# Performance work log

Hardware: AMD Instinct MI355X
Metric: run time of the kernel (lower is better)

Reference implementation:

```python
import jax, jax.numpy as jnp
import numpy as np

NN, D, H = 100000, 300, 1024   # nodes, embedding dim, hidden dim
NG, NS = 50000, 25000          # global vocab, sense vocab
B, T = 8, 128                  # batch, sequence length (state carried across all B*T steps)


def setup_inputs() -> dict:
    key = jax.random.key(0)
    ks = jax.random.split(key, 24)
    s = lambda i, shape: (jax.random.normal(ks[i], shape, jnp.float32) * 0.02)
    return {
        "x_idx": jax.random.randint(ks[0], (B, T), 0, NN),
        "X": jax.random.normal(ks[1], (NN, D), jnp.float32) * 0.1,
        "W_z_1": s(2, (D, H)), "U_z_1": s(3, (H, H)),
        "W_r_1": s(4, (D, H)), "U_r_1": s(5, (H, H)),
        "W_1": s(6, (D, H)), "b_W_1": jnp.zeros((H,), jnp.float32),
        "U_1": s(7, (H, H)), "b_U_1": jnp.zeros((H,), jnp.float32),
        "W_z_2": s(8, (H, H)), "U_z_2": s(9, (H, H)),
        "W_r_2": s(10, (H, H)), "U_r_2": s(11, (H, H)),
        "W_2": s(12, (H, H)), "b_W_2": jnp.zeros((H,), jnp.float32),
        "U_2": s(13, (H, H)), "b_U_2": jnp.zeros((H,), jnp.float32),
        "W_g": s(14, (H, NG)), "b_g": jnp.zeros((NG,), jnp.float32),
        "W_s": s(15, (H, NS)), "b_s": jnp.zeros((NS,), jnp.float32),
    }


def reference(x_idx, X, W_z_1, U_z_1, W_r_1, U_r_1, W_1, b_W_1, U_1, b_U_1,
              W_z_2, U_z_2, W_r_2, U_r_2, W_2, b_W_2, U_2, b_U_2,
              W_g, b_g, W_s, b_s):
    # The original loops over every sample of every sequence, carrying memory_h1/h2
    # across the whole batch; only X[x_indices[0]] feeds the GRU (the GAT-projected
    # neighbours are computed but never used). Dropout in eval mode = identity.
    idx = x_idx.reshape(-1)          # [S] flattened step order (seq-major per sample)
    emb = X[idx]                     # [S, D] currentword embeddings

    def step(carry, e):
        h1, h2 = carry
        z1 = jax.nn.sigmoid(e @ W_z_1 + h1 @ U_z_1)
        r1 = jax.nn.sigmoid(e @ W_r_1 + h1 @ U_r_1)
        ht1 = jnp.tanh((e @ W_1 + b_W_1) + ((r1 * h1) @ U_1 + b_U_1))
        h1n = z1 * ht1 + (1.0 - z1) * h1
        z2 = jax.nn.sigmoid(h1n @ W_z_2 + h2 @ U_z_2)
        r2 = jax.nn.sigmoid(h1n @ W_r_2 + h2 @ U_r_2)
        ht2 = jnp.tanh((h1n @ W_2 + b_W_2) + ((r2 * h2) @ U_2 + b_U_2))
        h2n = z2 * ht2 + (1.0 - z2) * h2
        return (h1n, h2n), h2n

    h0 = jnp.zeros((H,), emb.dtype)
    _, hs = jax.lax.scan(step, (h0, h0), emb)        # hs: [S, H]
    logp_g = jax.nn.log_softmax(hs @ W_g + b_g, axis=-1)   # [S, NG]
    logp_s = jax.nn.log_softmax(hs @ W_s + b_s, axis=-1)   # [S, NS]
    return logp_g, logp_s
```

## Files before the change

### kernel.cpp

```cpp
#include <hip/hip_runtime.h>

typedef __attribute__((ext_vector_type(4))) float f32x4;
typedef __attribute__((ext_vector_type(8))) __bf16 bf16x8;
typedef __attribute__((ext_vector_type(4))) unsigned short u16x4;

#define GPAD 40
#define KEEPF(x) asm volatile("" : "+v"(x))
#define PHYS(i) ((i) + (((i) >> 6) << 2))

__device__ unsigned long long g_h1s[1025 * 1024];
__device__ unsigned long long g_rh1[1024];
__device__ unsigned long long g_h2cur[1024];
__device__ unsigned long long g_rh2[1024];
__device__ float g_ExW[1024 * 3072];
__device__ float g_hs2[1024 * 1024];

__device__ __forceinline__ unsigned short f2bf(float x) {
  unsigned u = __builtin_bit_cast(unsigned, x);
  u += 0x7FFFu + ((u >> 16) & 1u);
  return (unsigned short)(u >> 16);
}
__device__ __forceinline__ unsigned long long packtv(unsigned tag, float v) {
  return ((unsigned long long)tag << 32) | (unsigned long long)__builtin_bit_cast(unsigned, v);
}
__device__ __forceinline__ unsigned long long aload(const unsigned long long* p) {
  return __hip_atomic_load(p, __ATOMIC_RELAXED, __HIP_MEMORY_SCOPE_AGENT);
}
__device__ __forceinline__ void astore(unsigned long long* p, unsigned long long v) {
  __hip_atomic_store(p, v, __ATOMIC_RELAXED, __HIP_MEMORY_SCOPE_AGENT);
}
__device__ __forceinline__ float lo32(unsigned long long v) {
  return __builtin_bit_cast(float, (unsigned)v);
}

__global__ void init_kernel() {
  int t = threadIdx.x;
  astore(&g_rh1[t], 0ull);
  astore(&g_h2cur[t], 0ull);
  astore(&g_rh2[t], 0ull);
}

__global__ __launch_bounds__(256, 1) void fused_scan(
    const float* __restrict__ ExW,
    const float* __restrict__ Uz1, const float* __restrict__ Ur1,
    const float* __restrict__ Uw1, const float* __restrict__ bU1,
    const float* __restrict__ Wz2, const float* __restrict__ Wr2,
    const float* __restrict__ Ww2,
    const float* __restrict__ Uz2, const float* __restrict__ Ur2,
    const float* __restrict__ Uw2,
    const float* __restrict__ bW2, const float* __restrict__ bU2,
    float* __restrict__ hs2)
{
  const int tid = threadIdx.x;
  const int wv = tid >> 6, inw = tid & 63;
  __shared__ __align__(16) float h_s[1088];
  __shared__ __align__(16) float rh_s[1088];
  __shared__ __align__(16) float x_s[1088];

  if (blockIdx.x < 64) {
    const int g = blockIdx.x;
    const int c2 = inw >> 4, q = inw & 15;
    const int j = g * 16 + wv * 4 + c2;
    float uz[64], ur[64], uw[64];
#pragma unroll
    for (int i = 0; i < 64; ++i) uz[i] = Uz1[(size_t)(q * 64 + i) * 1024 + j];
#pragma unroll
    for (int i = 0; i < 64; ++i) ur[i] = Ur1[(size_t)(q * 64 + i) * 1024 + j];
#pragma unroll
    for (int i = 0; i < 64; ++i) uw[i] = Uw1[(size_t)(q * 64 + i) * 1024 + j];
#pragma unroll
    for (int i = 0; i < 64; ++i) { KEEPF(uz[i]); KEEPF(ur[i]); KEEPF(uw[i]); }
    const float bu = bU1[j];

    float xz = 0.f, xr = 0.f, xw = 0.f;
    if (q == 0) { xz = ExW[j]; xr = ExW[1024 + j]; xw = ExW[2048 + j]; }

    float zreg = 0.f, hold = 0.f;
    for (int s = 0; s < 1024; ++s) {
      {
        const unsigned long long* sl = g_h1s + (size_t)s * 1024 + tid * 4;
        unsigned long long a0, a1, a2, a3;
        for (;;) {
          a0 = aload(sl); a1 = aload(sl + 1); a2 = aload(sl + 2); a3 = aload(sl + 3);
          unsigned bad = ((unsigned)(a0 >> 32) ^ (unsigned)s) | ((unsigned)(a1 >> 32) ^ (unsigned)s) |
                         ((unsigned)(a2 >> 32) ^ (unsigned)s) | ((unsigned)(a3 >> 32) ^ (unsigned)s);
          if (bad == 0u) break;
          __builtin_amdgcn_s_sleep(1);
        }
        f32x4 v; v.x = lo32(a0); v.y = lo32(a1); v.z = lo32(a2); v.w = lo32(a3);
        *(f32x4*)&h_s[PHYS(tid * 4)] = v;
      }
      __syncthreads();
      if (q == 0) hold = h_s[PHYS(j)];
      float ar_ = 0.f;
      {
        const float* hp = h_s + q * 68;
#pragma unroll
        for (int i2 = 0; i2 < 16; ++i2) {
          f32x4 hv = *(const f32x4*)(hp + i2 * 4);
          ar_ = fmaf(ur[i2 * 4 + 0], hv.x, ar_); ar_ = fmaf(ur[i2 * 4 + 1], hv.y, ar_);
          ar_ = fmaf(ur[i2 * 4 + 2], hv.z, ar_); ar_ = fmaf(ur[i2 * 4 + 3], hv.w, ar_);
        }
      }
      ar_ += __shfl_xor(ar_, 1, 64); ar_ += __shfl_xor(ar_, 2, 64);
      ar_ += __shfl_xor(ar_, 4, 64); ar_ += __shfl_xor(ar_, 8, 64);
      if (q == 0) {
        float r = 1.f / (1.f + __expf(-(ar_ + xr)));
        astore(&g_rh1[j], packtv((unsigned)(s + 1), r * hold));
      }
      float az_ = 0.f;
      {
        const float* hp = h_s + q * 68;
#pragma unroll
        for (int i2 = 0; i2 < 16; ++i2) {
          f32x4 hv = *(const f32x4*)(hp + i2 * 4);
          az_ = fmaf(uz[i2 * 4 + 0], hv.x, az_); az_ = fmaf(uz[i2 * 4 + 1], hv.y, az_);
          az_ = fmaf(uz[i2 * 4 + 2], hv.z, az_); az_ = fmaf(uz[i2 * 4 + 3], hv.w, az_);
        }
      }
      az_ += __shfl_xor(az_, 1, 64); az_ += __shfl_xor(az_, 2, 64);
      az_ += __shfl_xor(az_, 4, 64); az_ += __shfl_xor(az_, 8, 64);
      if (q == 0) zreg = 1.f / (1.f + __expf(-(az_ + xz)));
      float nxz = 0.f, nxr = 0.f, nxw = 0.f;
      if (q == 0 && s < 1023) {
        nxz = ExW[(s + 1) * 3072 + j];
        nxr = ExW[(s + 1) * 3072 + 1024 + j];
        nxw = ExW[(s + 1) * 3072 + 2048 + j];
      }
      {
        const unsigned long long* sl = g_rh1 + tid * 4;
        unsigned long long a0, a1, a2, a3;
        const unsigned tg = (unsigned)(s + 1);
        for (;;) {
          a0 = aload(sl); a1 = aload(sl + 1); a2 = aload(sl + 2); a3 = aload(sl + 3);
          unsigned bad = ((unsigned)(a0 >> 32) ^ tg) | ((unsigned)(a1 >> 32) ^ tg) |
                         ((unsigned)(a2 >> 32) ^ tg) | ((unsigned)(a3 >> 32) ^ tg);
          if (bad == 0u) break;
          __builtin_amdgcn_s_sleep(1);
        }
        f32x4 v; v.x = lo32(a0); v.y = lo32(a1); v.z = lo32(a2); v.w = lo32(a3);
        *(f32x4*)&rh_s[PHYS(tid * 4)] = v;
      }
      __syncthreads();
      float aw_ = 0.f;
      {
        const float* rp = rh_s + q * 68;
#pragma unroll
        for (int i2 = 0; i2 < 16; ++i2) {
          f32x4 rv = *(const f32x4*)(rp + i2 * 4);
          aw_ = fmaf(uw[i2 * 4 + 0], rv.x, aw_); aw_ = fmaf(uw[i2 * 4 + 1], rv.y, aw_);
          aw_ = fmaf(uw[i2 * 4 + 2], rv.z, aw_); aw_ = fmaf(uw[i2 * 4 + 3], rv.w, aw_);
        }
      }
      aw_ += __shfl_xor(aw_, 1, 64); aw_ += __shfl_xor(aw_, 2, 64);
      aw_ += __shfl_xor(aw_, 4, 64); aw_ += __shfl_xor(aw_, 8, 64);
      if (q == 0) {
        float ht = tanhf(aw_ + xw + bu);
        float hn = zreg * ht + (1.f - zreg) * hold;
        astore(&g_h1s[(size_t)(s + 1) * 1024 + j], packtv((unsigned)(s + 1), hn));
      }
      xz = nxz; xr = nxr; xw = nxw;
    }
  } else {
    const int g = blockIdx.x - 64;
    const int c2 = inw >> 5, q = inw & 31;
    const int j = g * 8 + wv * 2 + c2;
    const int sb = q * 32 + ((q >> 1) << 2);
    float uz[32], ur[32], uw[32], wz[32], wr[32], ww[32];
#pragma unroll
    for (int i = 0; i < 32; ++i) uz[i] = Uz2[(size_t)(q * 32 + i) * 1024 + j];
#pragma unroll
    for (int i = 0; i < 32; ++i) ur[i] = Ur2[(size_t)(q * 32 + i) * 1024 + j];
#pragma unroll
    for (int i = 0; i < 32; ++i) uw[i] = Uw2[(size_t)(q * 32 + i) * 1024 + j];
#pragma unroll
    for (int i = 0; i < 32; ++i) wz[i] = Wz2[(size_t)(q * 32 + i) * 1024 + j];
#pragma unroll
    for (int i = 0; i < 32; ++i) wr[i] = Wr2[(size_t)(q * 32 + i) * 1024 + j];
#pragma unroll
    for (int i = 0; i < 32; ++i) ww[i] = Ww2[(size_t)(q * 32 + i) * 1024 + j];
#pragma unroll
    for (int i = 0; i < 32; ++i) {
      KEEPF(uz[i]); KEEPF(ur[i]); KEEPF(uw[i]);
      KEEPF(wz[i]); KEEPF(wr[i]); KEEPF(ww[i]);
    }
    const float bu = bW2[j] + bU2[j];

    float zreg = 0.f, hold = 0.f;
    for (int s = 0; s < 1024; ++s) {
      {
        const unsigned long long* sh = g_h2cur + tid * 4;
        const unsigned long long* sx = g_h1s + (size_t)(s + 1) * 1024 + tid * 4;
        unsigned long long a0, a1, a2, a3, b0, b1, b2, b3;
        const unsigned tg = (unsigned)(s + 1);
        for (;;) {
          a0 = aload(sh); a1 = aload(sh + 1); a2 = aload(sh + 2); a3 = aload(sh + 3);
          b0 = aload(sx); b1 = aload(sx + 1); b2 = aload(sx + 2); b3 = aload(sx + 3);
          unsigned bad = ((unsigned)(a0 >> 32) ^ (unsigned)s) | ((unsigned)(a1 >> 32) ^ (unsigned)s) |
                         ((unsigned)(a2 >> 32) ^ (unsigned)s) | ((unsigned)(a3 >> 32) ^ (unsigned)s) |
                         ((unsigned)(b0 >> 32) ^ tg) | ((unsigned)(b1 >> 32) ^ tg) |
                         ((unsigned)(b2 >> 32) ^ tg) | ((unsigned)(b3 >> 32) ^ tg);
          if (bad == 0u) break;
          __builtin_amdgcn_s_sleep(1);
        }
        f32x4 v; v.x = lo32(a0); v.y = lo32(a1); v.z = lo32(a2); v.w = lo32(a3);
        *(f32x4*)&h_s[PHYS(tid * 4)] = v;
        f32x4 u4; u4.x = lo32(b0); u4.y = lo32(b1); u4.z = lo32(b2); u4.w = lo32(b3);
        *(f32x4*)&x_s[PHYS(tid * 4)] = u4;
      }
      __syncthreads();
      if (q == 0) hold = h_s[PHYS(j)];
      float ar_ = 0.f;
      {
        const float* hp = h_s + sb;
        const float* xp = x_s + sb;
#pragma unroll
        for (int i2 = 0; i2 < 8; ++i2) {
          f32x4 hv = *(const f32x4*)(hp + i2 * 4);
          f32x4 xv = *(const f32x4*)(xp + i2 * 4);
          ar_ = fmaf(ur[i2 * 4 + 0], hv.x, ar_); ar_ = fmaf(ur[i2 * 4 + 1], hv.y, ar_);
          ar_ = fmaf(ur[i2 * 4 + 2], hv.z, ar_); ar_ = fmaf(ur[i2 * 4 + 3], hv.w, ar_);
          ar_ = fmaf(wr[i2 * 4 + 0], xv.x, ar_); ar_ = fmaf(wr[i2 * 4 + 1], xv.y, ar_);
          ar_ = fmaf(wr[i2 * 4 + 2], xv.z, ar_); ar_ = fmaf(wr[i2 * 4 + 3], xv.w, ar_);
        }
      }
      ar_ += __shfl_xor(ar_, 1, 64); ar_ += __shfl_xor(ar_, 2, 64);
      ar_ += __shfl_xor(ar_, 4, 64); ar_ += __shfl_xor(ar_, 8, 64);
      ar_ += __shfl_xor(ar_, 16, 64);
      if (q == 0) {
        float r = 1.f / (1.f + __expf(-ar_));
        astore(&g_rh2[j], packtv((unsigned)(s + 1), r * hold));
      }
      float az_ = 0.f;
      {
        const float* hp = h_s + sb;
        const float* xp = x_s + sb;
#pragma unroll
        for (int i2 = 0; i2 < 8; ++i2) {
          f32x4 hv = *(const f32x4*)(hp + i2 * 4);
          f32x4 xv = *(const f32x4*)(xp + i2 * 4);
          az_ = fmaf(uz[i2 * 4 + 0], hv.x, az_); az_ = fmaf(uz[i2 * 4 + 1], hv.y, az_);
          az_ = fmaf(uz[i2 * 4 + 2], hv.z, az_); az_ = fmaf(uz[i2 * 4 + 3], hv.w, az_);
          az_ = fmaf(wz[i2 * 4 + 0], xv.x, az_); az_ = fmaf(wz[i2 * 4 + 1], xv.y, az_);
          az_ = fmaf(wz[i2 * 4 + 2], xv.z, az_); az_ = fmaf(wz[i2 * 4 + 3], xv.w, az_);
        }
      }
      az_ += __shfl_xor(az_, 1, 64); az_ += __shfl_xor(az_, 2, 64);
      az_ += __shfl_xor(az_, 4, 64); az_ += __shfl_xor(az_, 8, 64);
      az_ += __shfl_xor(az_, 16, 64);
      if (q == 0) zreg = 1.f / (1.f + __expf(-az_));
      {
        const unsigned long long* sl = g_rh2 + tid * 4;
        unsigned long long a0, a1, a2, a3;
        const unsigned tg = (unsigned)(s + 1);
        for (;;) {
          a0 = aload(sl); a1 = aload(sl + 1); a2 = aload(sl + 2); a3 = aload(sl + 3);
          unsigned bad = ((unsigned)(a0 >> 32) ^ tg) | ((unsigned)(a1 >> 32) ^ tg) |
                         ((unsigned)(a2 >> 32) ^ tg) | ((unsigned)(a3 >> 32) ^ tg);
          if (bad == 0u) break;
          __builtin_amdgcn_s_sleep(1);
        }
        f32x4 v; v.x = lo32(a0); v.y = lo32(a1); v.z = lo32(a2); v.w = lo32(a3);
        *(f32x4*)&rh_s[PHYS(tid * 4)] = v;
      }
      __syncthreads();
      float aw_ = 0.f;
      {
        const float* rp = rh_s + sb;
        const float* xp = x_s + sb;
#pragma unroll
        for (int i2 = 0; i2 < 8; ++i2) {
          f32x4 rv = *(const f32x4*)(rp + i2 * 4);
          f32x4 xv = *(const f32x4*)(xp + i2 * 4);
          aw_ = fmaf(uw[i2 * 4 + 0], rv.x, aw_); aw_ = fmaf(uw[i2 * 4 + 1], rv.y, aw_);
          aw_ = fmaf(uw[i2 * 4 + 2], rv.z, aw_); aw_ = fmaf(uw[i2 * 4 + 3], rv.w, aw_);
          aw_ = fmaf(ww[i2 * 4 + 0], xv.x, aw_); aw_ = fmaf(ww[i2 * 4 + 1], xv.y, aw_);
          aw_ = fmaf(ww[i2 * 4 + 2], xv.z, aw_); aw_ = fmaf(ww[i2 * 4 + 3], xv.w, aw_);
        }
      }
      aw_ += __shfl_xor(aw_, 1, 64); aw_ += __shfl_xor(aw_, 2, 64);
      aw_ += __shfl_xor(aw_, 4, 64); aw_ += __shfl_xor(aw_, 8, 64);
      aw_ += __shfl_xor(aw_, 16, 64);
      if (q == 0) {
        float ht = tanhf(aw_ + bu);
        float hn = zreg * ht + (1.f - zreg) * hold;
        astore(&g_h2cur[j], packtv((unsigned)(s + 1), hn));
        hs2[(size_t)s * 1024 + j] = hn;
      }
    }
  }
}

__global__ __launch_bounds__(256, 1) void gemm_mfma(
    const float* __restrict__ A, const int* __restrict__ gidx, int lda,
    const float* __restrict__ B, int ldb,
    const float* __restrict__ bias,
    float* __restrict__ C, int ldc, int N, int K)
{
  __shared__ unsigned short As[128 * GPAD];
  __shared__ unsigned short Bs[128 * GPAD];
  const int tid = threadIdx.x;
  const int lane = tid & 63;
  const int wv = tid >> 6;
  const int wm = wv >> 1, wn = wv & 1;
  const int mbase = blockIdx.y * 128, nbase = blockIdx.x * 128;

  f32x4 acc[4][4];
#pragma unroll
  for (int i = 0; i < 4; ++i)
#pragma unroll
    for (int qq = 0; qq < 4; ++qq) acc[i][qq] = (f32x4){0.f, 0.f, 0.f, 0.f};

  const int ar = tid >> 1, ak = (tid & 1) * 16;
  const float* Arow;
  {
    int m = mbase + ar;
    long long gr = gidx ? (long long)gidx[m] : (long long)m;
    Arow = A + (size_t)gr * (size_t)lda;
  }
  const int bn = (tid >> 3) * 4;
  const int bk = (tid & 7) * 4;
  const bool nedge = (nbase + 128 > N);

  const int ksteps = (K + 31) >> 5;
  for (int ks = 0; ks < ksteps; ++ks) {
    const int k0 = ks << 5;
    __syncthreads();
    {
      float v[16];
      const int kg = k0 + ak;
      if (kg + 16 <= K) {
#pragma unroll
        for (int qq = 0; qq < 4; ++qq) {
          f32x4 t = *(const f32x4*)(Arow + kg + qq * 4);
          v[qq * 4 + 0] = t.x; v[qq * 4 + 1] = t.y; v[qq * 4 + 2] = t.z; v[qq * 4 + 3] = t.w;
        }
      } else {
#pragma unroll
        for (int i = 0; i < 16; ++i) v[i] = (kg + i < K) ? Arow[kg + i] : 0.f;
      }
#pragma unroll
      for (int qq = 0; qq < 4; ++qq) {
        u16x4 wq;
        wq.x = f2bf(v[qq * 4 + 0]); wq.y = f2bf(v[qq * 4 + 1]);
        wq.z = f2bf(v[qq * 4 + 2]); wq.w = f2bf(v[qq * 4 + 3]);
        *(u16x4*)&As[ar * GPAD + ak + qq * 4] = wq;
      }
    }
    {
      float bv[4][4];
#pragma unroll
      for (int kk = 0; kk < 4; ++kk) {
        int kglob = k0 + bk + kk;
        if (kglob < K) {
          if (!nedge) {
            f32x4 t = *(const f32x4*)(B + (size_t)kglob * (size_t)ldb + nbase + bn);
            bv[kk][0] = t.x; bv[kk][1] = t.y; bv[kk][2] = t.z; bv[kk][3] = t.w;
          } else {
#pragma unroll
            for (int nn = 0; nn < 4; ++nn) {
              int n = nbase + bn + nn;
              bv[kk][nn] = (n < N) ? B[(size_t)kglob * (size_t)ldb + n] : 0.f;
            }
          }
        } else {
          bv[kk][0] = bv[kk][1] = bv[kk][2] = bv[kk][3] = 0.f;
        }
      }
#pragma unroll
      for (int nn = 0; nn < 4; ++nn) {
        u16x4 wq;
        wq.x = f2bf(bv[0][nn]); wq.y = f2bf(bv[1][nn]);
        wq.z = f2bf(bv[2][nn]); wq.w = f2bf(bv[3][nn]);
        *(u16x4*)&Bs[(bn + nn) * GPAD + bk] = wq;
      }
    }
    __syncthreads();
    bf16x8 af[4], bfr[4];
    const int fr = lane & 15, fk = (lane >> 4) * 8;
#pragma unroll
    for (int mf = 0; mf < 4; ++mf)
      af[mf] = *(const bf16x8*)&As[(wm * 64 + mf * 16 + fr) * GPAD + fk];
#pragma unroll
    for (int nf = 0; nf < 4; ++nf)
      bfr[nf] = *(const bf16x8*)&Bs[(wn * 64 + nf * 16 + fr) * GPAD + fk];
#pragma unroll
    for (int mf = 0; mf < 4; ++mf)
#pragma unroll
      for (int nf = 0; nf < 4; ++nf)
        acc[mf][nf] = __builtin_amdgcn_mfma_f32_16x16x32_bf16(af[mf], bfr[nf], acc[mf][nf], 0, 0, 0);
  }
  const int fr = lane & 15, fq = lane >> 4;
#pragma unroll
  for (int nf = 0; nf < 4; ++nf) {
    int col = nbase + wn * 64 + nf * 16 + fr;
    if (col < N) {
      float bb = bias ? bias[col] : 0.f;
#pragma unroll
      for (int mf = 0; mf < 4; ++mf) {
        int row0 = mbase + wm * 64 + mf * 16 + fq * 4;
#pragma unroll
        for (int r = 0; r < 4; ++r)
          C[(size_t)(row0 + r) * (size_t)ldc + col] = acc[mf][nf][r] + bb;
      }
    }
  }
}

__global__ __launch_bounds__(256, 1) void logsoftmax_kernel(float* __restrict__ out) {
  const int row = blockIdx.x;
  float* p; int len;
  if (row < 1024) { p = out + (size_t)row * 50000u; len = 50000; }
  else            { p = out + 51200000ull + (size_t)(row - 1024) * 25000u; len = 25000; }
  const int tid = threadIdx.x;
  __shared__ float mred[4], sred[4];

  float m = -3.4e38f;
  for (int i = tid * 4; i < len; i += 1024) {
    f32x4 v = *(const f32x4*)(p + i);
    m = fmaxf(m, fmaxf(fmaxf(v.x, v.y), fmaxf(v.z, v.w)));
  }
#pragma unroll
  for (int off = 32; off >= 1; off >>= 1) m = fmaxf(m, __shfl_xor(m, off, 64));
  if ((tid & 63) == 0) mred[tid >> 6] = m;
  __syncthreads();
  m = fmaxf(fmaxf(mred[0], mred[1]), fmaxf(mred[2], mred[3]));

  float ssum = 0.f;
  for (int i = tid * 4; i < len; i += 1024) {
    f32x4 v = *(const f32x4*)(p + i);
    ssum += __expf(v.x - m) + __expf(v.y - m) + __expf(v.z - m) + __expf(v.w - m);
  }
#pragma unroll
  for (int off = 32; off >= 1; off >>= 1) ssum += __shfl_xor(ssum, off, 64);
  if ((tid & 63) == 0) sred[tid >> 6] = ssum;
  __syncthreads();
  const float lse = m + logf(sred[0] + sred[1] + sred[2] + sred[3]);

  for (int i = tid * 4; i < len; i += 1024) {
    f32x4 v = *(const f32x4*)(p + i);
    v.x -= lse; v.y -= lse; v.z -= lse; v.w -= lse;
    *(f32x4*)(p + i) = v;
  }
}

extern "C" void kernel_launch(void* const* d_in, const int* in_sizes, int n_in,
                              void* d_out, int out_size, void* d_ws, size_t ws_size,
                              hipStream_t stream) {
  (void)in_sizes; (void)n_in; (void)out_size; (void)d_ws; (void)ws_size;
  const int*   x_idx = (const int*)  d_in[0];
  const float* X     = (const float*)d_in[1];
  const float* W_z_1 = (const float*)d_in[2];
  const float* U_z_1 = (const float*)d_in[3];
  const float* W_r_1 = (const float*)d_in[4];
  const float* U_r_1 = (const float*)d_in[5];
  const float* W_1   = (const float*)d_in[6];
  const float* b_W_1 = (const float*)d_in[7];
  const float* U_1   = (const float*)d_in[8];
  const float* b_U_1 = (const float*)d_in[9];
  const float* W_z_2 = (const float*)d_in[10];
  const float* U_z_2 = (const float*)d_in[11];
  const float* W_r_2 = (const float*)d_in[12];
  const float* U_r_2 = (const float*)d_in[13];
  const float* W_2   = (const float*)d_in[14];
  const float* b_W_2 = (const float*)d_in[15];
  const float* U_2   = (const float*)d_in[16];
  const float* b_U_2 = (const float*)d_in[17];
  const float* W_g   = (const float*)d_in[18];
  const float* b_g   = (const float*)d_in[19];
  const float* W_s   = (const float*)d_in[20];
  const float* b_s   = (const float*)d_in[21];
  float* out = (float*)d_out;

  float *ExW, *hs2;
  unsigned long long* h1s;
  hipGetSymbolAddress((void**)&ExW, HIP_SYMBOL(g_ExW));
  hipGetSymbolAddress((void**)&hs2, HIP_SYMBOL(g_hs2));
  hipGetSymbolAddress((void**)&h1s, HIP_SYMBOL(g_h1s));

  const dim3 blk(256);

  init_kernel<<<dim3(1), dim3(1024), 0, stream>>>();
  hipMemsetAsync(h1s, 0, 1025ull * 1024 * sizeof(unsigned long long), stream);

  gemm_mfma<<<dim3(8, 8), blk, 0, stream>>>(X, x_idx, 300, W_z_1, 1024, nullptr, ExW + 0,    3072, 1024, 300);
  gemm_mfma<<<dim3(8, 8), blk, 0, stream>>>(X, x_idx, 300, W_r_1, 1024, nullptr, ExW + 1024, 3072, 1024, 300);
  gemm_mfma<<<dim3(8, 8), blk, 0, stream>>>(X, x_idx, 300, W_1,   1024, b_W_1,   ExW + 2048, 3072, 1024, 300);

  fused_scan<<<dim3(192), blk, 0, stream>>>(
      ExW, U_z_1, U_r_1, U_1, b_U_1,
      W_z_2, W_r_2, W_2, U_z_2, U_r_2, U_2, b_W_2, b_U_2, hs2);

  gemm_mfma<<<dim3(391, 8), blk, 0, stream>>>(hs2, nullptr, 1024, W_g, 50000, b_g, out,              50000, 50000, 1024);
  gemm_mfma<<<dim3(196, 8), blk, 0, stream>>>(hs2, nullptr, 1024, W_s, 25000, b_s, out + 51200000ll, 25000, 25000, 1024);
  logsoftmax_kernel<<<dim3(2048), blk, 0, stream>>>(out);
}
```

Measured before the change: 6.803 ms.

## Gate scan phases on sharded per-wave completion counters instead of tag polling

Adds sharded global counters per phase that each wave increments after publishing its outputs. Consumers spin on a single counter per lane with __all before reading the tagged data, rather than polling the tagged arrays directly. Because the counters gate access, the large memset of the h1 history buffer is dropped and only row 0 is zeroed in init. The next-step ExW prefetch is moved after publishing h1. This is meant to cut polling traffic on the critical path and remove the memset, at the cost of extra atomics and waitcnt stalls per step.

```diff
diff --git a/kernel.cpp b/kernel.cpp
--- a/kernel.cpp
+++ b/kernel.cpp
@@ -7,11 +7,17 @@
 #define GPAD 40
 #define KEEPF(x) asm volatile("" : "+v"(x))
 #define PHYS(i) ((i) + (((i) >> 6) << 2))
+
+#define PH_H1  0
+#define PH_RH1 1
+#define PH_H2  2
+#define PH_RH2 3
 
 __device__ unsigned long long g_h1s[1025 * 1024];
 __device__ unsigned long long g_rh1[1024];
 __device__ unsigned long long g_h2cur[1024];
 __device__ unsigned long long g_rh2[1024];
+__device__ unsigned g_cnt[4 * 32 * 16];
 __device__ float g_ExW[1024 * 3072];
 __device__ float g_hs2[1024 * 1024];
 
@@ -29,8 +35,35 @@
 __device__ __forceinline__ void astore(unsigned long long* p, unsigned long long v) {
   __hip_atomic_store(p, v, __ATOMIC_RELAXED, __HIP_MEMORY_SCOPE_AGENT);
 }
+__device__ __forceinline__ unsigned cload(const unsigned* p) {
+  return __hip_atomic_load(p, __ATOMIC_RELAXED, __HIP_MEMORY_SCOPE_AGENT);
+}
 __device__ __forceinline__ float lo32(unsigned long long v) {
   return __builtin_bit_cast(float, (unsigned)v);
+}
+
+__device__ __forceinline__ void gate(int ph, unsigned thr, int inw) {
+  const unsigned* cp = &g_cnt[(ph * 32 + (inw & 31)) * 16];
+  for (;;) {
+    unsigned v = cload(cp);
+    if (__all((int)(v >= thr))) break;
+    __builtin_amdgcn_s_sleep(1);
+  }
+}
+__device__ __forceinline__ void gate2(int phA, unsigned thrA, int phB, unsigned thrB, int inw) {
+  const unsigned* ca = &g_cnt[(phA * 32 + (inw & 31)) * 16];
+  const unsigned* cb = &g_cnt[(phB * 32 + (inw & 31)) * 16];
+  for (;;) {
+    unsigned va = cload(ca), vb = cload(cb);
+    if (__all((int)((va >= thrA) && (vb >= thrB)))) break;
+    __builtin_amdgcn_s_sleep(1);
+  }
+}
+__device__ __forceinline__ void publish_done(int ph, int wid) {
+  asm volatile("s_waitcnt vmcnt(0)" ::: "memory");
+  if ((threadIdx.x & 63) == 0)
+    (void)__hip_atomic_fetch_add(&g_cnt[(ph * 32 + (wid & 31)) * 16], 1u,
+                                 __ATOMIC_RELAXED, __HIP_MEMORY_SCOPE_AGENT);
 }
 
 __global__ void init_kernel() {
@@ -38,6 +71,9 @@
   astore(&g_rh1[t], 0ull);
   astore(&g_h2cur[t], 0ull);
   astore(&g_rh2[t], 0ull);
+  astore(&g_h1s[t], 0ull);
+  __hip_atomic_store(&g_cnt[2 * t], 0u, __ATOMIC_RELAXED, __HIP_MEMORY_SCOPE_AGENT);
+  __hip_atomic_store(&g_cnt[2 * t + 1], 0u, __ATOMIC_RELAXED, __HIP_MEMORY_SCOPE_AGENT);
 }
 
 __global__ __launch_bounds__(256, 1) void fused_scan(
@@ -59,6 +95,7 @@
 
   if (blockIdx.x < 64) {
     const int g = blockIdx.x;
+    const int wid = g * 4 + wv;
     const int c2 = inw >> 4, q = inw & 15;
     const int j = g * 16 + wv * 4 + c2;
     float uz[64], ur[64], uw[64];
@@ -77,6 +114,7 @@
 
     float zreg = 0.f, hold = 0.f;
     for (int s = 0; s < 1024; ++s) {
+      gate(PH_H1, (unsigned)s << 3, inw);
       {
         const unsigned long long* sl = g_h1s + (size_t)s * 1024 + tid * 4;
         unsigned long long a0, a1, a2, a3;
@@ -108,6 +146,7 @@
         float r = 1.f / (1.f + __expf(-(ar_ + xr)));
         astore(&g_rh1[j], packtv((unsigned)(s + 1), r * hold));
       }
+      publish_done(PH_RH1, wid);
       float az_ = 0.f;
       {
         const float* hp = h_s + q * 68;
@@ -121,12 +160,7 @@
       az_ += __shfl_xor(az_, 1, 64); az_ += __shfl_xor(az_, 2, 64);
       az_ += __shfl_xor(az_, 4, 64); az_ += __shfl_xor(az_, 8, 64);
       if (q == 0) zreg = 1.f / (1.f + __expf(-(az_ + xz)));
-      float nxz = 0.f, nxr = 0.f, nxw = 0.f;
-      if (q == 0 && s < 1023) {
-        nxz = ExW[(s + 1) * 3072 + j];
-        nxr = ExW[(s + 1) * 3072 + 1024 + j];
-        nxw = ExW[(s + 1) * 3072 + 2048 + j];
-      }
+      gate(PH_RH1, (unsigned)(s + 1) << 3, inw);
       {
         const unsigned long long* sl = g_rh1 + tid * 4;
         unsigned long long a0, a1, a2, a3;
@@ -159,10 +193,18 @@
         float hn = zreg * ht + (1.f - zreg) * hold;
         astore(&g_h1s[(size_t)(s + 1) * 1024 + j], packtv((unsigned)(s + 1), hn));
       }
+      publish_done(PH_H1, wid);
+      float nxz = 0.f, nxr = 0.f, nxw = 0.f;
+      if (q == 0 && s < 1023) {
+        nxz = ExW[(s + 1) * 3072 + j];
+        nxr = ExW[(s + 1) * 3072 + 1024 + j];
+        nxw = ExW[(s + 1) * 3072 + 2048 + j];
+      }
       xz = nxz; xr = nxr; xw = nxw;
     }
   } else {
     const int g = blockIdx.x - 64;
+    const int wid = g * 4 + wv;
     const int c2 = inw >> 5, q = inw & 31;
     const int j = g * 8 + wv * 2 + c2;
     const int sb = q * 32 + ((q >> 1) << 2);
@@ -188,6 +230,7 @@
 
     float zreg = 0.f, hold = 0.f;
     for (int s = 0; s < 1024; ++s) {
+      gate2(PH_H2, (unsigned)s << 4, PH_H1, (unsigned)(s + 1) << 3, inw);
       {
         const unsigned long long* sh = g_h2cur + tid * 4;
         const unsigned long long* sx = g_h1s + (size_t)(s + 1) * 1024 + tid * 4;
@@ -231,6 +274,7 @@
         float r = 1.f / (1.f + __expf(-ar_));
         astore(&g_rh2[j], packtv((unsigned)(s + 1), r * hold));
       }
+      publish_done(PH_RH2, wid);
       float az_ = 0.f;
       {
         const float* hp = h_s + sb;
@@ -249,6 +293,7 @@
       az_ += __shfl_xor(az_, 4, 64); az_ += __shfl_xor(az_, 8, 64);
       az_ += __shfl_xor(az_, 16, 64);
       if (q == 0) zreg = 1.f / (1.f + __expf(-az_));
+      gate(PH_RH2, (unsigned)(s + 1) << 4, inw);
       {
         const unsigned long long* sl = g_rh2 + tid * 4;
         unsigned long long a0, a1, a2, a3;
@@ -287,6 +332,7 @@
         astore(&g_h2cur[j], packtv((unsigned)(s + 1), hn));
         hs2[(size_t)s * 1024 + j] = hn;
       }
+      publish_done(PH_H2, wid);
     }
   }
 }
@@ -473,15 +519,12 @@
   float* out = (float*)d_out;
 
   float *ExW, *hs2;
-  unsigned long long* h1s;
   hipGetSymbolAddress((void**)&ExW, HIP_SYMBOL(g_ExW));
   hipGetSymbolAddress((void**)&hs2, HIP_SYMBOL(g_hs2));
-  hipGetSymbolAddress((void**)&h1s, HIP_SYMBOL(g_h1s));
 
   const dim3 blk(256);
 
   init_kernel<<<dim3(1), dim3(1024), 0, stream>>>();
-  hipMemsetAsync(h1s, 0, 1025ull * 1024 * sizeof(unsigned long long), stream);
 
   gemm_mfma<<<dim3(8, 8), blk, 0, stream>>>(X, x_idx, 300, W_z_1, 1024, nullptr, ExW + 0,    3072, 1024, 300);
   gemm_mfma<<<dim3(8, 8), blk, 0, stream>>>(X, x_idx, 300, W_r_1, 1024, nullptr, ExW + 1024, 3072, 1024, 300);
```

After: 12.82 ms. 88.5% more time.

## Replicate recurrent state into per-block mailboxes to localize spin-wait polling

Applied to the files above, without the earlier changes.

Each producer now writes its hidden-state and reset-gated values into a separate mailbox copy for every consumer block. Consumers therefore poll a private contiguous slot instead of all blocks hammering one shared array. The aim is to cut cache-line contention and coherence traffic in the cross-block handshake that runs on every recurrent step. The cost is 64–128x more atomic stores per step, a larger zero-init memset, and the next-step ExW prefetch moving to after the publish; layer-2 sleep duration is also raised.

```diff
diff --git a/kernel.cpp b/kernel.cpp
--- a/kernel.cpp
+++ b/kernel.cpp
@@ -8,12 +8,15 @@
 #define KEEPF(x) asm volatile("" : "+v"(x))
 #define PHYS(i) ((i) + (((i) >> 6) << 2))
 
+__device__ unsigned long long g_mb[384 * 1024];
 __device__ unsigned long long g_h1s[1025 * 1024];
-__device__ unsigned long long g_rh1[1024];
-__device__ unsigned long long g_h2cur[1024];
-__device__ unsigned long long g_rh2[1024];
 __device__ float g_ExW[1024 * 3072];
 __device__ float g_hs2[1024 * 1024];
+
+#define MB_H1  0
+#define MB_RH1 (64 * 1024)
+#define MB_H2  (128 * 1024)
+#define MB_RH2 (256 * 1024)
 
 __device__ __forceinline__ unsigned short f2bf(float x) {
   unsigned u = __builtin_bit_cast(unsigned, x);
@@ -31,13 +34,6 @@
 }
 __device__ __forceinline__ float lo32(unsigned long long v) {
   return __builtin_bit_cast(float, (unsigned)v);
-}
-
-__global__ void init_kernel() {
-  int t = threadIdx.x;
-  astore(&g_rh1[t], 0ull);
-  astore(&g_h2cur[t], 0ull);
-  astore(&g_rh2[t], 0ull);
 }
 
 __global__ __launch_bounds__(256, 1) void fused_scan(
@@ -72,13 +68,16 @@
     for (int i = 0; i < 64; ++i) { KEEPF(uz[i]); KEEPF(ur[i]); KEEPF(uw[i]); }
     const float bu = bU1[j];
 
+    const int pv_ = inw & 3, pm0 = inw >> 2;
+    unsigned long long* const pubj = g_mb + (size_t)(g * 16 + wv * 4 + pv_);
+
     float xz = 0.f, xr = 0.f, xw = 0.f;
     if (q == 0) { xz = ExW[j]; xr = ExW[1024 + j]; xw = ExW[2048 + j]; }
 
     float zreg = 0.f, hold = 0.f;
     for (int s = 0; s < 1024; ++s) {
       {
-        const unsigned long long* sl = g_h1s + (size_t)s * 1024 + tid * 4;
+        const unsigned long long* sl = g_mb + MB_H1 + g * 1024 + tid * 4;
         unsigned long long a0, a1, a2, a3;
         for (;;) {
           a0 = aload(sl); a1 = aload(sl + 1); a2 = aload(sl + 2); a3 = aload(sl + 3);
@@ -104,9 +103,19 @@
       }
       ar_ += __shfl_xor(ar_, 1, 64); ar_ += __shfl_xor(ar_, 2, 64);
       ar_ += __shfl_xor(ar_, 4, 64); ar_ += __shfl_xor(ar_, 8, 64);
+      float rhv = 0.f;
       if (q == 0) {
         float r = 1.f / (1.f + __expf(-(ar_ + xr)));
-        astore(&g_rh1[j], packtv((unsigned)(s + 1), r * hold));
+        rhv = r * hold;
+      }
+      {
+        float pvv = __shfl(rhv, pv_ * 16, 64);
+        unsigned long long pk = packtv((unsigned)(s + 1), pvv);
+        unsigned long long* b = pubj + MB_RH1;
+        astore(b + (size_t)pm0 * 1024, pk);
+        astore(b + (size_t)(pm0 + 16) * 1024, pk);
+        astore(b + (size_t)(pm0 + 32) * 1024, pk);
+        astore(b + (size_t)(pm0 + 48) * 1024, pk);
       }
       float az_ = 0.f;
       {
@@ -121,14 +130,8 @@
       az_ += __shfl_xor(az_, 1, 64); az_ += __shfl_xor(az_, 2, 64);
       az_ += __shfl_xor(az_, 4, 64); az_ += __shfl_xor(az_, 8, 64);
       if (q == 0) zreg = 1.f / (1.f + __expf(-(az_ + xz)));
-      float nxz = 0.f, nxr = 0.f, nxw = 0.f;
-      if (q == 0 && s < 1023) {
-        nxz = ExW[(s + 1) * 3072 + j];
-        nxr = ExW[(s + 1) * 3072 + 1024 + j];
-        nxw = ExW[(s + 1) * 3072 + 2048 + j];
-      }
-      {
-        const unsigned long long* sl = g_rh1 + tid * 4;
+      {
+        const unsigned long long* sl = g_mb + MB_RH1 + g * 1024 + tid * 4;
         unsigned long long a0, a1, a2, a3;
         const unsigned tg = (unsigned)(s + 1);
         for (;;) {
@@ -154,10 +157,26 @@
       }
       aw_ += __shfl_xor(aw_, 1, 64); aw_ += __shfl_xor(aw_, 2, 64);
       aw_ += __shfl_xor(aw_, 4, 64); aw_ += __shfl_xor(aw_, 8, 64);
+      float hn = 0.f;
       if (q == 0) {
         float ht = tanhf(aw_ + xw + bu);
-        float hn = zreg * ht + (1.f - zreg) * hold;
-        astore(&g_h1s[(size_t)(s + 1) * 1024 + j], packtv((unsigned)(s + 1), hn));
+        hn = zreg * ht + (1.f - zreg) * hold;
+      }
+      {
+        float pvv = __shfl(hn, pv_ * 16, 64);
+        unsigned long long pk = packtv((unsigned)(s + 1), pvv);
+        unsigned long long* b = pubj + MB_H1;
+        astore(b + (size_t)pm0 * 1024, pk);
+        astore(b + (size_t)(pm0 + 16) * 1024, pk);
+        astore(b + (size_t)(pm0 + 32) * 1024, pk);
+        astore(b + (size_t)(pm0 + 48) * 1024, pk);
+        if (q == 0) astore(&g_h1s[(size_t)(s + 1) * 1024 + j], pk);
+      }
+      float nxz = 0.f, nxr = 0.f, nxw = 0.f;
+      if (q == 0 && s < 1023) {
+        nxz = ExW[(s + 1) * 3072 + j];
+        nxr = ExW[(s + 1) * 3072 + 1024 + j];
+        nxw = ExW[(s + 1) * 3072 + 2048 + j];
       }
       xz = nxz; xr = nxr; xw = nxw;
     }
@@ -186,10 +205,13 @@
     }
     const float bu = bW2[j] + bU2[j];
 
+    const int pv_ = inw & 1, pm0 = inw >> 1;
+    unsigned long long* const pubj = g_mb + (size_t)(g * 8 + wv * 2 + pv_);
+
     float zreg = 0.f, hold = 0.f;
     for (int s = 0; s < 1024; ++s) {
       {
-        const unsigned long long* sh = g_h2cur + tid * 4;
+        const unsigned long long* sh = g_mb + MB_H2 + g * 1024 + tid * 4;
         const unsigned long long* sx = g_h1s + (size_t)(s + 1) * 1024 + tid * 4;
         unsigned long long a0, a1, a2, a3, b0, b1, b2, b3;
         const unsigned tg = (unsigned)(s + 1);
@@ -201,7 +223,7 @@
                          ((unsigned)(b0 >> 32) ^ tg) | ((unsigned)(b1 >> 32) ^ tg) |
                          ((unsigned)(b2 >> 32) ^ tg) | ((unsigned)(b3 >> 32) ^ tg);
           if (bad == 0u) break;
-          __builtin_amdgcn_s_sleep(1);
+          __builtin_amdgcn_s_sleep(2);
         }
         f32x4 v; v.x = lo32(a0); v.y = lo32(a1); v.z = lo32(a2); v.w = lo32(a3);
         *(f32x4*)&h_s[PHYS(tid * 4)] = v;
@@ -227,9 +249,19 @@
       ar_ += __shfl_xor(ar_, 1, 64); ar_ += __shfl_xor(ar_, 2, 64);
       ar_ += __shfl_xor(ar_, 4, 64); ar_ += __shfl_xor(ar_, 8, 64);
       ar_ += __shfl_xor(ar_, 16, 64);
+      float rhv = 0.f;
       if (q == 0) {
         float r = 1.f / (1.f + __expf(-ar_));
-        astore(&g_rh2[j], packtv((unsigned)(s + 1), r * hold));
+        rhv = r * hold;
+      }
+      {
+        float pvv = __shfl(rhv, pv_ * 32, 64);
+        unsigned long long pk = packtv((unsigned)(s + 1), pvv);
+        unsigned long long* b = pubj + MB_RH2;
+        astore(b + (size_t)pm0 * 1024, pk);
+        astore(b + (size_t)(pm0 + 32) * 1024, pk);
+        astore(b + (size_t)(pm0 + 64) * 1024, pk);
+        astore(b + (size_t)(pm0 + 96) * 1024, pk);
       }
       float az_ = 0.f;
       {
@@ -250,7 +282,7 @@
       az_ += __shfl_xor(az_, 16, 64);
       if (q == 0) zreg = 1.f / (1.f + __expf(-az_));
       {
-        const unsigned long long* sl = g_rh2 + tid * 4;
+        const unsigned long long* sl = g_mb + MB_RH2 + g * 1024 + tid * 4;
         unsigned long long a0, a1, a2, a3;
         const unsigned tg = (unsigned)(s + 1);
         for (;;) {
@@ -281,11 +313,20 @@
       aw_ += __shfl_xor(aw_, 1, 64); aw_ += __shfl_xor(aw_, 2, 64);
       aw_ += __shfl_xor(aw_, 4, 64); aw_ += __shfl_xor(aw_, 8, 64);
       aw_ += __shfl_xor(aw_, 16, 64);
+      float hn = 0.f;
       if (q == 0) {
         float ht = tanhf(aw_ + bu);
-        float hn = zreg * ht + (1.f - zreg) * hold;
-        astore(&g_h2cur[j], packtv((unsigned)(s + 1), hn));
+        hn = zreg * ht + (1.f - zreg) * hold;
         hs2[(size_t)s * 1024 + j] = hn;
+      }
+      {
+        float pvv = __shfl(hn, pv_ * 32, 64);
+        unsigned long long pk = packtv((unsigned)(s + 1), pvv);
+        unsigned long long* b = pubj + MB_H2;
+        astore(b + (size_t)pm0 * 1024, pk);
+        astore(b + (size_t)(pm0 + 32) * 1024, pk);
+        astore(b + (size_t)(pm0 + 64) * 1024, pk);
+        astore(b + (size_t)(pm0 + 96) * 1024, pk);
       }
     }
   }
@@ -473,14 +514,15 @@
   float* out = (float*)d_out;
 
   float *ExW, *hs2;
-  unsigned long long* h1s;
+  unsigned long long *mb, *h1s;
   hipGetSymbolAddress((void**)&ExW, HIP_SYMBOL(g_ExW));
   hipGetSymbolAddress((void**)&hs2, HIP_SYMBOL(g_hs2));
+  hipGetSymbolAddress((void**)&mb, HIP_SYMBOL(g_mb));
   hipGetSymbolAddress((void**)&h1s, HIP_SYMBOL(g_h1s));
 
   const dim3 blk(256);
 
-  init_kernel<<<dim3(1), dim3(1024), 0, stream>>>();
+  hipMemsetAsync(mb, 0, 384ull * 1024 * sizeof(unsigned long long), stream);
   hipMemsetAsync(h1s, 0, 1025ull * 1024 * sizeof(unsigned long long), stream);
 
   gemm_mfma<<<dim3(8, 8), blk, 0, stream>>>(X, x_idx, 300, W_z_1, 1024, nullptr, ExW + 0,    3072, 1024, 300);
```

After: 9.445 ms. +38.8%, slower.
